# Optimization experiments

Measured on AMD Instinct MI355X. Metric: run time of the kernel, lower is better.

Reference implementation:

```python
import jax, jax.numpy as jnp
import numpy as np

NUM_HEADS = 8
MODEL_DIM = 512
HIDDEN_DIM = 64  # model_dim // num_heads
BATCH = 4
SEQ = 1024


def setup_inputs() -> dict:
    key = jax.random.key(0)
    kx, kq, kk, kv, ko = jax.random.split(key, 5)
    # xavier_uniform bound for [model_dim, hidden_dim] fan pair
    bqkv = float(np.sqrt(6.0 / (MODEL_DIM + HIDDEN_DIM)))
    bo = float(np.sqrt(6.0 / (MODEL_DIM + MODEL_DIM)))
    return {
        "X": jax.random.normal(kx, (BATCH, SEQ, MODEL_DIM), dtype=jnp.float32),
        "mask": jnp.zeros((SEQ, SEQ), dtype=bool),  # unused by module
        "Wq": jax.random.uniform(kq, (NUM_HEADS, MODEL_DIM, HIDDEN_DIM), minval=-bqkv, maxval=bqkv, dtype=jnp.float32),
        "Wk": jax.random.uniform(kk, (NUM_HEADS, MODEL_DIM, HIDDEN_DIM), minval=-bqkv, maxval=bqkv, dtype=jnp.float32),
        "Wv": jax.random.uniform(kv, (NUM_HEADS, MODEL_DIM, HIDDEN_DIM), minval=-bqkv, maxval=bqkv, dtype=jnp.float32),
        "Wo": jax.random.uniform(ko, (MODEL_DIM, MODEL_DIM), minval=-bo, maxval=bo, dtype=jnp.float32),
    }


def reference(X, mask, Wq, Wk, Wv, Wo):
    # Per-head projections (replaces the replicated-tensor lin_proj with one einsum)
    q = jnp.einsum("bsm,hmd->hbsd", X, Wq)  # [h,b,s,d]
    k = jnp.einsum("bsm,hmd->hbsd", X, Wk)
    v = jnp.einsum("bsm,hmd->hbsd", X, Wv)
    # Katharopoulos feature map on q and k
    q = jax.nn.elu(q) + 1.0
    k = jax.nn.elu(k) + 1.0
    # Cumulative outer-product state S_t = sum_{i<=t} k_i v_i^T  -> [h,b,s,d,d]
    S = jnp.cumsum(k[..., :, None] * v[..., None, :], axis=2)
    V_bar = jnp.einsum("hbsd,hbsde->hbse", q, S)  # numerator
    Z = jnp.einsum("hbsd,hbsd->hbs", q, jnp.cumsum(k, axis=2))  # normalizer
    out_heads = V_bar / Z[..., None]  # [h,b,s,d]
    # combine_heads: permute to [b,s,h,d], flatten heads, project by Wo
    b, s = out_heads.shape[1], out_heads.shape[2]
    combined = jnp.transpose(out_heads, (1, 2, 0, 3)).reshape(b, s, -1)
    return jnp.einsum("bsm,mn->bsn", combined, Wo)
```

## Files before the change

kernel.cpp:

```cpp
#include <hip/hip_runtime.h>
#include <math.h>

namespace {
typedef unsigned short u16;
typedef __attribute__((ext_vector_type(8))) short bf16x8;
typedef __attribute__((ext_vector_type(4))) float f32x4;

constexpr int H  = 8;
constexpr int B  = 4;
constexpr int S  = 1024;
constexpr int M  = 512;
constexpr int D  = 64;
constexpr int BS = B * S;
constexpr int NC = 16;
constexpr int CH = 64;
constexpr int QSZ = H * B * S * D;
constexpr int NQKV = 3 * M;

__device__ __forceinline__ float elu1(float x) {
  return x > 0.f ? x + 1.f : __expf(x);
}

__device__ __forceinline__ u16 f2bf(float f) {
  unsigned u = __builtin_bit_cast(unsigned, f);
  u += 0x7fffu + ((u >> 16) & 1u);
  return (u16)(u >> 16);
}

__device__ __forceinline__ float bf2f(u16 v) {
  return __builtin_bit_cast(float, ((unsigned)v) << 16);
}

__device__ __forceinline__ void gload16(const u16* g, u16* l) {
  __builtin_amdgcn_global_load_lds(
      (const __attribute__((address_space(1))) unsigned int*)g,
      (__attribute__((address_space(3))) unsigned int*)l, 16, 0, 0);
}

__global__ __launch_bounds__(256) void prep(
    const float* __restrict__ X, const float* __restrict__ Wq,
    const float* __restrict__ Wk, const float* __restrict__ Wv,
    const float* __restrict__ Wo, u16* __restrict__ Xb,
    u16* __restrict__ WCT, u16* __restrict__ WoT) {
  __shared__ float t[64][65];
  const int bid = blockIdx.x;
  if (bid < 2048) {
    const int i = bid * 256 + threadIdx.x;
    const float4 v = reinterpret_cast<const float4*>(X)[i];
    u16 o[4] = {f2bf(v.x), f2bf(v.y), f2bf(v.z), f2bf(v.w)};
    *reinterpret_cast<uint2*>(Xb + i * 4) = *reinterpret_cast<uint2*>(o);
  } else if (bid < 2240) {
    const int bb = bid - 2048;
    const int mt = bb & 7, ph = bb >> 3;
    const int p = ph >> 3, h = ph & 7;
    const float* W = ((p == 0) ? Wq : (p == 1) ? Wk : Wv) + h * (M * D);
    const int m0 = mt * 64;
#pragma unroll
    for (int j = 0; j < 4; ++j) {
      const int i = j * 256 + threadIdx.x;
      const int mm = i >> 4, dd = (i & 15) * 4;
      const float4 v = *reinterpret_cast<const float4*>(W + (m0 + mm) * D + dd);
      t[mm][dd + 0] = v.x; t[mm][dd + 1] = v.y;
      t[mm][dd + 2] = v.z; t[mm][dd + 3] = v.w;
    }
    __syncthreads();
    const int dd = threadIdx.x >> 2, qr = (threadIdx.x & 3) * 16;
    u16* o = WCT + (p * M + h * D + dd) * M + m0 + qr;
#pragma unroll
    for (int i = 0; i < 16; ++i) o[i] = f2bf(t[qr + i][dd]);
  } else {
    const int bb = bid - 2240;
    const int m0 = (bb & 7) * 64, n0 = (bb >> 3) * 64;
#pragma unroll
    for (int j = 0; j < 4; ++j) {
      const int i = j * 256 + threadIdx.x;
      const int mm = i >> 4, nn = (i & 15) * 4;
      const float4 v = *reinterpret_cast<const float4*>(Wo + (m0 + mm) * M + n0 + nn);
      t[mm][nn + 0] = v.x; t[mm][nn + 1] = v.y;
      t[mm][nn + 2] = v.z; t[mm][nn + 3] = v.w;
    }
    __syncthreads();
    const int nn = threadIdx.x >> 2, qr = (threadIdx.x & 3) * 16;
    u16* o = WoT + (n0 + nn) * M + m0 + qr;
#pragma unroll
    for (int i = 0; i < 16; ++i) o[i] = f2bf(t[qr + i][nn]);
  }
}

__global__ __launch_bounds__(256) void gemm_qkv(const u16* __restrict__ A,
                                                const u16* __restrict__ BT,
                                                u16* __restrict__ qb,
                                                u16* __restrict__ kb,
                                                u16* __restrict__ kTb,
                                                u16* __restrict__ vTb) {
  __shared__ alignas(16) u16 As[2][4096];
  __shared__ alignas(16) u16 Bs[2][4096];
  const int tid = threadIdx.x;
  const int wave = tid >> 6, lane = tid & 63;
  const int r0 = blockIdx.x * 128, c0 = blockIdx.y * 128;
  const int wr = (wave >> 1) * 64, wc = (wave & 1) * 64;

  f32x4 acc[4][4] = {};
  const int lrow = tid >> 2;
  const int lk = (tid & 3) * 8;
  const u16* ga0 = A + (size_t)(r0 + lrow) * 512 + lk;
  const u16* ga1 = A + (size_t)(r0 + 64 + lrow) * 512 + lk;
  const u16* gb0 = BT + (size_t)(c0 + lrow) * 512 + lk;
  const u16* gb1 = BT + (size_t)(c0 + 64 + lrow) * 512 + lk;

#define STG_QKV(kt, b)                                \
  {                                                   \
    const int ko = (kt) * 32;                         \
    gload16(ga0 + ko, &As[b][wave * 512]);            \
    gload16(ga1 + ko, &As[b][2048 + wave * 512]);     \
    gload16(gb0 + ko, &Bs[b][wave * 512]);            \
    gload16(gb1 + ko, &Bs[b][2048 + wave * 512]);     \
  }

  STG_QKV(0, 0);
  __syncthreads();
  for (int kt = 0; kt < 16; ++kt) {
    if (kt < 15) STG_QKV(kt + 1, (kt + 1) & 1);
    const bf16x8* As8 = reinterpret_cast<const bf16x8*>(As[kt & 1]);
    const bf16x8* Bs8 = reinterpret_cast<const bf16x8*>(Bs[kt & 1]);
    bf16x8 af[4], bff[4];
#pragma unroll
    for (int mf = 0; mf < 4; ++mf)
      af[mf] = As8[(wr + mf * 16 + (lane & 15)) * 4 + (lane >> 4)];
#pragma unroll
    for (int nf = 0; nf < 4; ++nf)
      bff[nf] = Bs8[(wc + nf * 16 + (lane & 15)) * 4 + (lane >> 4)];
#pragma unroll
    for (int mf = 0; mf < 4; ++mf)
#pragma unroll
      for (int nf = 0; nf < 4; ++nf)
        acc[mf][nf] = __builtin_amdgcn_mfma_f32_16x16x32_bf16(
            af[mf], bff[nf], acc[mf][nf], 0, 0, 0);
    __syncthreads();
  }
#undef STG_QKV

#pragma unroll
  for (int nf = 0; nf < 4; ++nf) {
    const int col = c0 + wc + nf * 16 + (lane & 15);
    const int p = col >> 9, hh = (col >> 6) & 7, dd = col & 63;
#pragma unroll
    for (int mf = 0; mf < 4; ++mf) {
      const int rowb = r0 + wr + mf * 16 + (lane >> 4) * 4;
      const int b = rowb >> 10, s = rowb & 1023;
      const int hb = hh * B + b;
      u16 ov[4];
#pragma unroll
      for (int r = 0; r < 4; ++r) {
        float v = acc[mf][nf][r];
        if (p < 2) v = elu1(v);
        ov[r] = f2bf(v);
      }
      if (p == 0) {
#pragma unroll
        for (int r = 0; r < 4; ++r)
          qb[((size_t)(hb << 10) + s + r) * 64 + dd] = ov[r];
      } else if (p == 1) {
#pragma unroll
        for (int r = 0; r < 4; ++r)
          kb[((size_t)(hb << 10) + s + r) * 64 + dd] = ov[r];
        *reinterpret_cast<uint2*>(kTb + ((size_t)(hb * 64 + dd) << 10) + s) =
            *reinterpret_cast<uint2*>(ov);
      } else {
        *reinterpret_cast<uint2*>(vTb + ((size_t)(hb * 64 + dd) << 10) + s) =
            *reinterpret_cast<uint2*>(ov);
      }
    }
  }
}

__global__ __launch_bounds__(256) void gemm_out(const u16* __restrict__ A,
                                                const u16* __restrict__ BT,
                                                float* __restrict__ out) {
  __shared__ alignas(16) u16 As[2][4096];
  __shared__ alignas(16) u16 Bs[2][2048];
  const int tid = threadIdx.x;
  const int wave = tid >> 6, lane = tid & 63;
  const int r0 = blockIdx.x * 128, c0 = blockIdx.y * 64;
  const int wr = (wave >> 1) * 64, wc = (wave & 1) * 32;

  f32x4 acc[4][2] = {};
  const int lrow = tid >> 2;
  const int lk = (tid & 3) * 8;
  const u16* ga0 = A + (size_t)(r0 + lrow) * 512 + lk;
  const u16* ga1 = A + (size_t)(r0 + 64 + lrow) * 512 + lk;
  const u16* gb0 = BT + (size_t)(c0 + lrow) * 512 + lk;

#define STG_OUT(kt, b)                                \
  {                                                   \
    const int ko = (kt) * 32;                         \
    gload16(ga0 + ko, &As[b][wave * 512]);            \
    gload16(ga1 + ko, &As[b][2048 + wave * 512]);     \
    if (wave < 4) gload16(gb0 + ko, &Bs[b][wave * 512]); \
  }

  STG_OUT(0, 0);
  __syncthreads();
  for (int kt = 0; kt < 16; ++kt) {
    if (kt < 15) STG_OUT(kt + 1, (kt + 1) & 1);
    const bf16x8* As8 = reinterpret_cast<const bf16x8*>(As[kt & 1]);
    const bf16x8* Bs8 = reinterpret_cast<const bf16x8*>(Bs[kt & 1]);
    bf16x8 a[4], b[2];
#pragma unroll
    for (int mf = 0; mf < 4; ++mf)
      a[mf] = As8[(wr + mf * 16 + (lane & 15)) * 4 + (lane >> 4)];
#pragma unroll
    for (int nf = 0; nf < 2; ++nf)
      b[nf] = Bs8[(wc + nf * 16 + (lane & 15)) * 4 + (lane >> 4)];
#pragma unroll
    for (int mf = 0; mf < 4; ++mf)
#pragma unroll
      for (int nf = 0; nf < 2; ++nf)
        acc[mf][nf] = __builtin_amdgcn_mfma_f32_16x16x32_bf16(
            a[mf], b[nf], acc[mf][nf], 0, 0, 0);
    __syncthreads();
  }
#undef STG_OUT

#pragma unroll
  for (int nf = 0; nf < 2; ++nf) {
    const int col = c0 + wc + nf * 16 + (lane & 15);
#pragma unroll
    for (int mf = 0; mf < 4; ++mf)
#pragma unroll
      for (int r = 0; r < 4; ++r) {
        const int row = r0 + wr + mf * 16 + (lane >> 4) * 4 + r;
        out[(size_t)row * M + col] = acc[mf][nf][r];
      }
  }
}

__global__ __launch_bounds__(256) void chunkstate_mfma(
    const u16* __restrict__ kTb, const u16* __restrict__ vTb,
    float* __restrict__ G32, float* __restrict__ Ks) {
  const int tid = threadIdx.x, wave = tid >> 6, lane = tid & 63;
  const int bx = blockIdx.x, hb = bx >> 4, cc = bx & 15, s0 = cc * CH;
  const u16* vbase = vTb + ((size_t)hb * 64) * 1024 + s0;
  const u16* kbase = kTb + ((size_t)hb * 64) * 1024 + s0;

  bf16x8 av[2];
#pragma unroll
  for (int ks = 0; ks < 2; ++ks)
    av[ks] = *reinterpret_cast<const bf16x8*>(
        vbase + (size_t)(wave * 16 + (lane & 15)) * 1024 + ks * 32 + (lane >> 4) * 8);

  f32x4 acc[4] = {};
#pragma unroll
  for (int fd = 0; fd < 4; ++fd)
#pragma unroll
    for (int ks = 0; ks < 2; ++ks) {
      bf16x8 bk = *reinterpret_cast<const bf16x8*>(
          kbase + (size_t)(fd * 16 + (lane & 15)) * 1024 + ks * 32 + (lane >> 4) * 8);
      acc[fd] = __builtin_amdgcn_mfma_f32_16x16x32_bf16(av[ks], bk, acc[fd], 0, 0, 0);
    }

  float* Gp = G32 + (size_t)bx * 4096;
#pragma unroll
  for (int fd = 0; fd < 4; ++fd)
#pragma unroll
    for (int r = 0; r < 4; ++r) {
      const int e = wave * 16 + (lane >> 4) * 4 + r;
      const int d = fd * 16 + (lane & 15);
      Gp[e * 64 + d] = acc[fd][r];
    }

  const int d = tid >> 2, tq = tid & 3;
  const u16* kp = kbase + (size_t)d * 1024 + tq * 16;
  float ks = 0.f;
#pragma unroll
  for (int j = 0; j < 16; ++j) ks += bf2f(kp[j]);
  ks += __shfl_xor(ks, 1);
  ks += __shfl_xor(ks, 2);
  if (tq == 0) Ks[bx * 64 + d] = ks;
}

__global__ __launch_bounds__(256) void prefix_kernel(
    const float* __restrict__ G32, u16* __restrict__ GTb,
    float* __restrict__ Ks) {
  const int hb = blockIdx.x, eg = blockIdx.y;
  const int tid = threadIdx.x;
  const int e = eg * 4 + (tid >> 6), d = tid & 63;
  const size_t base = ((size_t)(hb * 16) * 64 + e) * 64 + d;
  float acc = 0.f;
#pragma unroll
  for (int c = 0; c < 16; ++c) {
    const float v = G32[base + (size_t)c * 4096];
    GTb[base + (size_t)c * 4096] = f2bf(acc);
    acc += v;
  }
  if (eg == 0 && tid < 64) {
    float ka = 0.f;
#pragma unroll
    for (int c = 0; c < 16; ++c) {
      const int idx = (hb * 16 + c) * 64 + tid;
      const float v = Ks[idx];
      Ks[idx] = ka;
      ka += v;
    }
  }
}

__global__ __launch_bounds__(256) void chunkout_mfma(
    const u16* __restrict__ qb, const u16* __restrict__ kb,
    const u16* __restrict__ vTb, const u16* __restrict__ GTb,
    const float* __restrict__ Kc, u16* __restrict__ att) {
  __shared__ alignas(16) u16 Qs[4096], Kls[4096], Vs[4096], Gs[4096], Astg[4096];
  const int tid = threadIdx.x, wave = tid >> 6, lane = tid & 63;
  const int bx = blockIdx.x, hb = bx >> 4, cc = bx & 15, s0 = cc * CH;
  const int h = hb >> 2, b = hb & 3;

  {
    const u16* qg = qb + ((size_t)(hb << 10) + s0) * 64;
    const u16* kg = kb + ((size_t)(hb << 10) + s0) * 64;
    const u16* gg = GTb + (size_t)bx * 4096;
#pragma unroll
    for (int j = 0; j < 2; ++j) {
      const int off = j * 2048 + wave * 512;
      gload16(qg + off + lane * 8, Qs + off);
      gload16(kg + off + lane * 8, Kls + off);
      gload16(gg + off + lane * 8, Gs + off);
    }
    const u16* vg = vTb + ((size_t)hb * 64) * 1024 + s0;
#pragma unroll
    for (int j = 0; j < 2; ++j) {
      const int e0 = j * 32 + wave * 8;
      gload16(vg + (size_t)(e0 + (lane >> 3)) * 1024 + (lane & 7) * 8,
              Vs + e0 * 64);
    }
  }
  __syncthreads();

  const bf16x8* Qs8 = reinterpret_cast<const bf16x8*>(Qs);
  const bf16x8* Ks8 = reinterpret_cast<const bf16x8*>(Kls);
  const bf16x8* Vs8 = reinterpret_cast<const bf16x8*>(Vs);
  const bf16x8* Gs8 = reinterpret_cast<const bf16x8*>(Gs);
  const bf16x8* As8 = reinterpret_cast<const bf16x8*>(Astg);

  const int i0 = wave * 16;
  const int l15 = lane & 15, lk = lane >> 4;

  bf16x8 aq[2];
#pragma unroll
  for (int ks = 0; ks < 2; ++ks)
    aq[ks] = Qs8[(i0 + l15) * 8 + ks * 4 + lk];

  f32x4 a[4] = {};
#pragma unroll
  for (int fj = 0; fj < 4; ++fj)
#pragma unroll
    for (int ks = 0; ks < 2; ++ks) {
      bf16x8 bk = Ks8[(fj * 16 + l15) * 8 + ks * 4 + lk];
      a[fj] = __builtin_amdgcn_mfma_f32_16x16x32_bf16(aq[ks], bk, a[fj], 0, 0, 0);
    }

  const float4 kc4 = *reinterpret_cast<const float4*>(Kc + bx * 64 + l15 * 4);
  float z[4];
  const int rbase = lk * 4;
#pragma unroll
  for (int r = 0; r < 4; ++r) {
    const int il = rbase + r;
    float sum = 0.f;
#pragma unroll
    for (int fj = 0; fj < 4; ++fj) {
      const int j = fj * 16 + l15;
      if (j > i0 + il) a[fj][r] = 0.f;
      sum += a[fj][r];
    }
    const uint2 qrow = *reinterpret_cast<const uint2*>(Qs + (i0 + il) * 64 + l15 * 4);
    const u16* qr16 = reinterpret_cast<const u16*>(&qrow);
    sum += bf2f(qr16[0]) * kc4.x + bf2f(qr16[1]) * kc4.y +
           bf2f(qr16[2]) * kc4.z + bf2f(qr16[3]) * kc4.w;
    z[r] = sum;
  }
#pragma unroll
  for (int off = 1; off <= 8; off <<= 1)
#pragma unroll
    for (int r = 0; r < 4; ++r) z[r] += __shfl_xor(z[r], off);

#pragma unroll
  for (int fj = 0; fj < 4; ++fj)
#pragma unroll
    for (int r = 0; r < 4; ++r)
      Astg[(i0 + rbase + r) * 64 + fj * 16 + l15] = f2bf(a[fj][r]);

  f32x4 o[4] = {};
#pragma unroll
  for (int fe = 0; fe < 4; ++fe) {
#pragma unroll
    for (int ks = 0; ks < 2; ++ks) {
      bf16x8 bg = Gs8[(fe * 16 + l15) * 8 + ks * 4 + lk];
      o[fe] = __builtin_amdgcn_mfma_f32_16x16x32_bf16(aq[ks], bg, o[fe], 0, 0, 0);
    }
#pragma unroll
    for (int ks = 0; ks < 2; ++ks) {
      bf16x8 aa = As8[(i0 + l15) * 8 + ks * 4 + lk];
      bf16x8 bv = Vs8[(fe * 16 + l15) * 8 + ks * 4 + lk];
      o[fe] = __builtin_amdgcn_mfma_f32_16x16x32_bf16(aa, bv, o[fe], 0, 0, 0);
    }
  }

  float rz[4];
#pragma unroll
  for (int r = 0; r < 4; ++r) rz[r] = 1.f / z[r];
#pragma unroll
  for (int fe = 0; fe < 4; ++fe)
#pragma unroll
    for (int r = 0; r < 4; ++r) {
      const int srow = s0 + i0 + rbase + r;
      att[((size_t)(b << 10) + srow) * 512 + h * 64 + fe * 16 + l15] =
          f2bf(o[fe][r] * rz[r]);
    }
}

}

extern "C" void kernel_launch(void* const* d_in, const int* in_sizes, int n_in,
                              void* d_out, int out_size, void* d_ws,
                              size_t ws_size, hipStream_t stream) {
  const float* X  = (const float*)d_in[0];
  const float* Wq = (const float*)d_in[2];
  const float* Wk = (const float*)d_in[3];
  const float* Wv = (const float*)d_in[4];
  const float* Wo = (const float*)d_in[5];
  float* out = (float*)d_out;

  u16* Xb  = (u16*)d_ws;
  u16* att = Xb;
  u16* WCT = Xb + QSZ;
  u16* WoT = WCT + NQKV * M;
  u16* qb  = WoT + M * M;
  u16* kb  = qb + QSZ;
  u16* kTb = kb + QSZ;
  u16* vTb = kTb + QSZ;
  u16* GTb = vTb + QSZ;
  float* G32 = (float*)(GTb + QSZ);
  float* Ks  = G32 + QSZ;

  prep<<<dim3(2304), 256, 0, stream>>>(X, Wq, Wk, Wv, Wo, Xb, WCT, WoT);
  gemm_qkv<<<dim3(BS / 128, NQKV / 128), 256, 0, stream>>>(Xb, WCT, qb, kb,
                                                           kTb, vTb);
  chunkstate_mfma<<<dim3(H * B * NC), 256, 0, stream>>>(kTb, vTb, G32, Ks);
  prefix_kernel<<<dim3(H * B, 16), 256, 0, stream>>>(G32, GTb, Ks);
  chunkout_mfma<<<dim3(H * B * NC), 256, 0, stream>>>(qb, kb, vTb, GTb, Ks,
                                                      att);
  gemm_out<<<dim3(BS / 128, M / 64), 256, 0, stream>>>(att, WoT, out);
}
```

Before: 52.63 us.

## Fold chunk prefix sum into chunkout and widen GEMM K-tiles with swizzled LDS

Removes the separate prefix_kernel launch: chunkstate now writes per-chunk states as bf16, and each chunkout block sums the preceding chunk states and key sums itself before its main work. Both projection GEMMs switch to 64-wide K tiles with an XOR-swizzled LDS layout, halving loop iterations and reducing bank conflicts. This drops one kernel launch and the fp32 state round trip, at the cost of redundant prefix work in later chunks (up to 15 state reads per block) and extra rounding, since states are stored in bf16 before being summed.

```diff
diff --git a/kernel.cpp b/kernel.cpp
--- a/kernel.cpp
+++ b/kernel.cpp
@@ -93,60 +93,64 @@
                                                 u16* __restrict__ kb,
                                                 u16* __restrict__ kTb,
                                                 u16* __restrict__ vTb) {
-  __shared__ alignas(16) u16 As[2][4096];
-  __shared__ alignas(16) u16 Bs[2][4096];
-  const int tid = threadIdx.x;
-  const int wave = tid >> 6, lane = tid & 63;
+  __shared__ alignas(16) u16 As[2][8192];
+  __shared__ alignas(16) u16 Bs[2][8192];
+  const int tid = threadIdx.x, wave = tid >> 6, lane = tid & 63;
   const int r0 = blockIdx.x * 128, c0 = blockIdx.y * 128;
   const int wr = (wave >> 1) * 64, wc = (wave & 1) * 64;
+  const int l15 = lane & 15, lk = lane >> 4, x7 = l15 & 7;
+  const int srow = wave * 8 + (lane >> 3);
+  const int scol = (((lane & 7) ^ ((lane >> 3) & 7)) * 8);
 
   f32x4 acc[4][4] = {};
-  const int lrow = tid >> 2;
-  const int lk = (tid & 3) * 8;
-  const u16* ga0 = A + (size_t)(r0 + lrow) * 512 + lk;
-  const u16* ga1 = A + (size_t)(r0 + 64 + lrow) * 512 + lk;
-  const u16* gb0 = BT + (size_t)(c0 + lrow) * 512 + lk;
-  const u16* gb1 = BT + (size_t)(c0 + 64 + lrow) * 512 + lk;
-
-#define STG_QKV(kt, b)                                \
-  {                                                   \
-    const int ko = (kt) * 32;                         \
-    gload16(ga0 + ko, &As[b][wave * 512]);            \
-    gload16(ga1 + ko, &As[b][2048 + wave * 512]);     \
-    gload16(gb0 + ko, &Bs[b][wave * 512]);            \
-    gload16(gb1 + ko, &Bs[b][2048 + wave * 512]);     \
+
+#define STG_QKV(kt, bb)                                                     \
+  {                                                                         \
+    const int k0 = (kt) * 64;                                               \
+    for (int j = 0; j < 4; ++j) {                                           \
+      gload16(A + (size_t)(r0 + j * 32 + srow) * 512 + k0 + scol,           \
+              &As[bb][j * 2048 + wave * 512]);                              \
+      gload16(BT + (size_t)(c0 + j * 32 + srow) * 512 + k0 + scol,          \
+              &Bs[bb][j * 2048 + wave * 512]);                              \
+    }                                                                       \
   }
 
   STG_QKV(0, 0);
   __syncthreads();
-  for (int kt = 0; kt < 16; ++kt) {
-    if (kt < 15) STG_QKV(kt + 1, (kt + 1) & 1);
+  for (int kt = 0; kt < 8; ++kt) {
+    if (kt < 7) STG_QKV(kt + 1, (kt + 1) & 1);
     const bf16x8* As8 = reinterpret_cast<const bf16x8*>(As[kt & 1]);
     const bf16x8* Bs8 = reinterpret_cast<const bf16x8*>(Bs[kt & 1]);
-    bf16x8 af[4], bff[4];
+    bf16x8 af[4][2], bf_[4][2];
 #pragma unroll
     for (int mf = 0; mf < 4; ++mf)
-      af[mf] = As8[(wr + mf * 16 + (lane & 15)) * 4 + (lane >> 4)];
+#pragma unroll
+      for (int ks = 0; ks < 2; ++ks)
+        af[mf][ks] = As8[(wr + mf * 16 + l15) * 8 + ((ks * 4 + lk) ^ x7)];
 #pragma unroll
     for (int nf = 0; nf < 4; ++nf)
-      bff[nf] = Bs8[(wc + nf * 16 + (lane & 15)) * 4 + (lane >> 4)];
-#pragma unroll
-    for (int mf = 0; mf < 4; ++mf)
-#pragma unroll
-      for (int nf = 0; nf < 4; ++nf)
-        acc[mf][nf] = __builtin_amdgcn_mfma_f32_16x16x32_bf16(
-            af[mf], bff[nf], acc[mf][nf], 0, 0, 0);
+#pragma unroll
+      for (int ks = 0; ks < 2; ++ks)
+        bf_[nf][ks] = Bs8[(wc + nf * 16 + l15) * 8 + ((ks * 4 + lk) ^ x7)];
+#pragma unroll
+    for (int ks = 0; ks < 2; ++ks)
+#pragma unroll
+      for (int mf = 0; mf < 4; ++mf)
+#pragma unroll
+        for (int nf = 0; nf < 4; ++nf)
+          acc[mf][nf] = __builtin_amdgcn_mfma_f32_16x16x32_bf16(
+              af[mf][ks], bf_[nf][ks], acc[mf][nf], 0, 0, 0);
     __syncthreads();
   }
 #undef STG_QKV
 
 #pragma unroll
   for (int nf = 0; nf < 4; ++nf) {
-    const int col = c0 + wc + nf * 16 + (lane & 15);
+    const int col = c0 + wc + nf * 16 + l15;
     const int p = col >> 9, hh = (col >> 6) & 7, dd = col & 63;
 #pragma unroll
     for (int mf = 0; mf < 4; ++mf) {
-      const int rowb = r0 + wr + mf * 16 + (lane >> 4) * 4;
+      const int rowb = r0 + wr + mf * 16 + lk * 4;
       const int b = rowb >> 10, s = rowb & 1023;
       const int hb = hh * B + b;
       u16 ov[4];
@@ -177,59 +181,65 @@
 __global__ __launch_bounds__(256) void gemm_out(const u16* __restrict__ A,
                                                 const u16* __restrict__ BT,
                                                 float* __restrict__ out) {
-  __shared__ alignas(16) u16 As[2][4096];
-  __shared__ alignas(16) u16 Bs[2][2048];
-  const int tid = threadIdx.x;
-  const int wave = tid >> 6, lane = tid & 63;
+  __shared__ alignas(16) u16 As[2][8192];
+  __shared__ alignas(16) u16 Bs[2][4096];
+  const int tid = threadIdx.x, wave = tid >> 6, lane = tid & 63;
   const int r0 = blockIdx.x * 128, c0 = blockIdx.y * 64;
   const int wr = (wave >> 1) * 64, wc = (wave & 1) * 32;
+  const int l15 = lane & 15, lk = lane >> 4, x7 = l15 & 7;
+  const int srow = wave * 8 + (lane >> 3);
+  const int scol = (((lane & 7) ^ ((lane >> 3) & 7)) * 8);
 
   f32x4 acc[4][2] = {};
-  const int lrow = tid >> 2;
-  const int lk = (tid & 3) * 8;
-  const u16* ga0 = A + (size_t)(r0 + lrow) * 512 + lk;
-  const u16* ga1 = A + (size_t)(r0 + 64 + lrow) * 512 + lk;
-  const u16* gb0 = BT + (size_t)(c0 + lrow) * 512 + lk;
-
-#define STG_OUT(kt, b)                                \
-  {                                                   \
-    const int ko = (kt) * 32;                         \
-    gload16(ga0 + ko, &As[b][wave * 512]);            \
-    gload16(ga1 + ko, &As[b][2048 + wave * 512]);     \
-    if (wave < 4) gload16(gb0 + ko, &Bs[b][wave * 512]); \
+
+#define STG_OUT(kt, bb)                                                     \
+  {                                                                         \
+    const int k0 = (kt) * 64;                                               \
+    for (int j = 0; j < 4; ++j)                                             \
+      gload16(A + (size_t)(r0 + j * 32 + srow) * 512 + k0 + scol,           \
+              &As[bb][j * 2048 + wave * 512]);                              \
+    for (int j = 0; j < 2; ++j)                                             \
+      gload16(BT + (size_t)(c0 + j * 32 + srow) * 512 + k0 + scol,          \
+              &Bs[bb][j * 2048 + wave * 512]);                              \
   }
 
   STG_OUT(0, 0);
   __syncthreads();
-  for (int kt = 0; kt < 16; ++kt) {
-    if (kt < 15) STG_OUT(kt + 1, (kt + 1) & 1);
+  for (int kt = 0; kt < 8; ++kt) {
+    if (kt < 7) STG_OUT(kt + 1, (kt + 1) & 1);
     const bf16x8* As8 = reinterpret_cast<const bf16x8*>(As[kt & 1]);
     const bf16x8* Bs8 = reinterpret_cast<const bf16x8*>(Bs[kt & 1]);
-    bf16x8 a[4], b[2];
+    bf16x8 a[4][2], b[2][2];
 #pragma unroll
     for (int mf = 0; mf < 4; ++mf)
-      a[mf] = As8[(wr + mf * 16 + (lane & 15)) * 4 + (lane >> 4)];
+#pragma unroll
+      for (int ks = 0; ks < 2; ++ks)
+        a[mf][ks] = As8[(wr + mf * 16 + l15) * 8 + ((ks * 4 + lk) ^ x7)];
 #pragma unroll
     for (int nf = 0; nf < 2; ++nf)
-      b[nf] = Bs8[(wc + nf * 16 + (lane & 15)) * 4 + (lane >> 4)];
+#pragma unroll
+      for (int ks = 0; ks < 2; ++ks)
+        b[nf][ks] = Bs8[(wc + nf * 16 + l15) * 8 + ((ks * 4 + lk) ^ x7)];
+#pragma unroll
+    for (int ks = 0; ks < 2; ++ks)
+#pragma unroll
+      for (int mf = 0; mf < 4; ++mf)
+#pragma unroll
+        for (int nf = 0; nf < 2; ++nf)
+          acc[mf][nf] = __builtin_amdgcn_mfma_f32_16x16x32_bf16(
+              a[mf][ks], b[nf][ks], acc[mf][nf], 0, 0, 0);
+    __syncthreads();
+  }
+#undef STG_OUT
+
+#pragma unroll
+  for (int nf = 0; nf < 2; ++nf) {
+    const int col = c0 + wc + nf * 16 + l15;
 #pragma unroll
     for (int mf = 0; mf < 4; ++mf)
 #pragma unroll
-      for (int nf = 0; nf < 2; ++nf)
-        acc[mf][nf] = __builtin_amdgcn_mfma_f32_16x16x32_bf16(
-            a[mf], b[nf], acc[mf][nf], 0, 0, 0);
-    __syncthreads();
-  }
-#undef STG_OUT
-
-#pragma unroll
-  for (int nf = 0; nf < 2; ++nf) {
-    const int col = c0 + wc + nf * 16 + (lane & 15);
-#pragma unroll
-    for (int mf = 0; mf < 4; ++mf)
-#pragma unroll
       for (int r = 0; r < 4; ++r) {
-        const int row = r0 + wr + mf * 16 + (lane >> 4) * 4 + r;
+        const int row = r0 + wr + mf * 16 + lk * 4 + r;
         out[(size_t)row * M + col] = acc[mf][nf][r];
       }
   }
@@ -237,17 +247,18 @@
 
 __global__ __launch_bounds__(256) void chunkstate_mfma(
     const u16* __restrict__ kTb, const u16* __restrict__ vTb,
-    float* __restrict__ G32, float* __restrict__ Ks) {
+    u16* __restrict__ Gb, float* __restrict__ Ks) {
   const int tid = threadIdx.x, wave = tid >> 6, lane = tid & 63;
   const int bx = blockIdx.x, hb = bx >> 4, cc = bx & 15, s0 = cc * CH;
   const u16* vbase = vTb + ((size_t)hb * 64) * 1024 + s0;
   const u16* kbase = kTb + ((size_t)hb * 64) * 1024 + s0;
+  const int l15 = lane & 15, lk = lane >> 4;
 
   bf16x8 av[2];
 #pragma unroll
   for (int ks = 0; ks < 2; ++ks)
     av[ks] = *reinterpret_cast<const bf16x8*>(
-        vbase + (size_t)(wave * 16 + (lane & 15)) * 1024 + ks * 32 + (lane >> 4) * 8);
+        vbase + (size_t)(wave * 16 + l15) * 1024 + ks * 32 + lk * 8);
 
   f32x4 acc[4] = {};
 #pragma unroll
@@ -255,19 +266,16 @@
 #pragma unroll
     for (int ks = 0; ks < 2; ++ks) {
       bf16x8 bk = *reinterpret_cast<const bf16x8*>(
-          kbase + (size_t)(fd * 16 + (lane & 15)) * 1024 + ks * 32 + (lane >> 4) * 8);
+          kbase + (size_t)(fd * 16 + l15) * 1024 + ks * 32 + lk * 8);
       acc[fd] = __builtin_amdgcn_mfma_f32_16x16x32_bf16(av[ks], bk, acc[fd], 0, 0, 0);
     }
 
-  float* Gp = G32 + (size_t)bx * 4096;
+  u16* Gp = Gb + (size_t)bx * 4096;
 #pragma unroll
   for (int fd = 0; fd < 4; ++fd)
 #pragma unroll
-    for (int r = 0; r < 4; ++r) {
-      const int e = wave * 16 + (lane >> 4) * 4 + r;
-      const int d = fd * 16 + (lane & 15);
-      Gp[e * 64 + d] = acc[fd][r];
-    }
+    for (int r = 0; r < 4; ++r)
+      Gp[(wave * 16 + lk * 4 + r) * 64 + fd * 16 + l15] = f2bf(acc[fd][r]);
 
   const int d = tid >> 2, tq = tid & 3;
   const u16* kp = kbase + (size_t)d * 1024 + tq * 16;
@@ -279,37 +287,12 @@
   if (tq == 0) Ks[bx * 64 + d] = ks;
 }
 
-__global__ __launch_bounds__(256) void prefix_kernel(
-    const float* __restrict__ G32, u16* __restrict__ GTb,
-    float* __restrict__ Ks) {
-  const int hb = blockIdx.x, eg = blockIdx.y;
-  const int tid = threadIdx.x;
-  const int e = eg * 4 + (tid >> 6), d = tid & 63;
-  const size_t base = ((size_t)(hb * 16) * 64 + e) * 64 + d;
-  float acc = 0.f;
-#pragma unroll
-  for (int c = 0; c < 16; ++c) {
-    const float v = G32[base + (size_t)c * 4096];
-    GTb[base + (size_t)c * 4096] = f2bf(acc);
-    acc += v;
-  }
-  if (eg == 0 && tid < 64) {
-    float ka = 0.f;
-#pragma unroll
-    for (int c = 0; c < 16; ++c) {
-      const int idx = (hb * 16 + c) * 64 + tid;
-      const float v = Ks[idx];
-      Ks[idx] = ka;
-      ka += v;
-    }
-  }
-}
-
 __global__ __launch_bounds__(256) void chunkout_mfma(
     const u16* __restrict__ qb, const u16* __restrict__ kb,
-    const u16* __restrict__ vTb, const u16* __restrict__ GTb,
-    const float* __restrict__ Kc, u16* __restrict__ att) {
+    const u16* __restrict__ vTb, const u16* __restrict__ Gb,
+    const float* __restrict__ Ks, u16* __restrict__ att) {
   __shared__ alignas(16) u16 Qs[4096], Kls[4096], Vs[4096], Gs[4096], Astg[4096];
+  __shared__ float Kcs[64];
   const int tid = threadIdx.x, wave = tid >> 6, lane = tid & 63;
   const int bx = blockIdx.x, hb = bx >> 4, cc = bx & 15, s0 = cc * CH;
   const int h = hb >> 2, b = hb & 3;
@@ -317,13 +300,11 @@
   {
     const u16* qg = qb + ((size_t)(hb << 10) + s0) * 64;
     const u16* kg = kb + ((size_t)(hb << 10) + s0) * 64;
-    const u16* gg = GTb + (size_t)bx * 4096;
 #pragma unroll
     for (int j = 0; j < 2; ++j) {
       const int off = j * 2048 + wave * 512;
       gload16(qg + off + lane * 8, Qs + off);
       gload16(kg + off + lane * 8, Kls + off);
-      gload16(gg + off + lane * 8, Gs + off);
     }
     const u16* vg = vTb + ((size_t)hb * 64) * 1024 + s0;
 #pragma unroll
@@ -331,6 +312,32 @@
       const int e0 = j * 32 + wave * 8;
       gload16(vg + (size_t)(e0 + (lane >> 3)) * 1024 + (lane & 7) * 8,
               Vs + e0 * 64);
+    }
+  }
+
+  {
+    const u16* gch = Gb + (size_t)(hb * 16) * 4096;
+    float gacc[16];
+#pragma unroll
+    for (int j = 0; j < 16; ++j) gacc[j] = 0.f;
+    for (int c = 0; c < cc; ++c) {
+      const bf16x8 g0 = *reinterpret_cast<const bf16x8*>(gch + (size_t)c * 4096 + tid * 16);
+      const bf16x8 g1 = *reinterpret_cast<const bf16x8*>(gch + (size_t)c * 4096 + tid * 16 + 8);
+#pragma unroll
+      for (int j = 0; j < 8; ++j) {
+        gacc[j] += bf2f((u16)g0[j]);
+        gacc[8 + j] += bf2f((u16)g1[j]);
+      }
+    }
+    u16 gq[16];
+#pragma unroll
+    for (int j = 0; j < 16; ++j) gq[j] = f2bf(gacc[j]);
+    *reinterpret_cast<uint4*>(Gs + tid * 16) = *reinterpret_cast<uint4*>(gq);
+    *reinterpret_cast<uint4*>(Gs + tid * 16 + 8) = *reinterpret_cast<uint4*>(gq + 8);
+    if (tid < 64) {
+      float kc = 0.f;
+      for (int c = 0; c < cc; ++c) kc += Ks[(hb * 16 + c) * 64 + tid];
+      Kcs[tid] = kc;
     }
   }
   __syncthreads();
@@ -358,7 +365,7 @@
       a[fj] = __builtin_amdgcn_mfma_f32_16x16x32_bf16(aq[ks], bk, a[fj], 0, 0, 0);
     }
 
-  const float4 kc4 = *reinterpret_cast<const float4*>(Kc + bx * 64 + l15 * 4);
+  const float4 kc4 = *reinterpret_cast<const float4*>(Kcs + l15 * 4);
   float z[4];
   const int rbase = lk * 4;
 #pragma unroll
@@ -437,16 +444,14 @@
   u16* kb  = qb + QSZ;
   u16* kTb = kb + QSZ;
   u16* vTb = kTb + QSZ;
-  u16* GTb = vTb + QSZ;
-  float* G32 = (float*)(GTb + QSZ);
-  float* Ks  = G32 + QSZ;
+  u16* Gb  = vTb + QSZ;
+  float* Ks = (float*)(Gb + QSZ);
 
   prep<<<dim3(2304), 256, 0, stream>>>(X, Wq, Wk, Wv, Wo, Xb, WCT, WoT);
   gemm_qkv<<<dim3(BS / 128, NQKV / 128), 256, 0, stream>>>(Xb, WCT, qb, kb,
                                                            kTb, vTb);
-  chunkstate_mfma<<<dim3(H * B * NC), 256, 0, stream>>>(kTb, vTb, G32, Ks);
-  prefix_kernel<<<dim3(H * B, 16), 256, 0, stream>>>(G32, GTb, Ks);
-  chunkout_mfma<<<dim3(H * B * NC), 256, 0, stream>>>(qb, kb, vTb, GTb, Ks,
+  chunkstate_mfma<<<dim3(H * B * NC), 256, 0, stream>>>(kTb, vTb, Gb, Ks);
+  chunkout_mfma<<<dim3(H * B * NC), 256, 0, stream>>>(qb, kb, vTb, Gb, Ks,
                                                       att);
   gemm_out<<<dim3(BS / 128, M / 64), 256, 0, stream>>>(att, WoT, out);
 }
```

Result: slower. 55.08 us (+4.7%).

## Triple-buffer LDS staging in QKV and output GEMMs with one barrier per step

Applied to the files above, without the earlier changes.

Both GEMM kernels go from double to triple buffering in shared memory. Loads now run two k-steps ahead and each step waits on a partial vmcnt. One barrier per iteration replaces two __syncthreads, which is meant to hide global-load latency and cut synchronisation. The cost is 50% more LDS per block, which may lower occupancy. The hand-written vmcnt counts also depend on exactly how the compiler emits the async loads. The always-true wave<4 guard was also dropped.

```diff
diff --git a/kernel.cpp b/kernel.cpp
--- a/kernel.cpp
+++ b/kernel.cpp
@@ -93,8 +93,8 @@
                                                 u16* __restrict__ kb,
                                                 u16* __restrict__ kTb,
                                                 u16* __restrict__ vTb) {
-  __shared__ alignas(16) u16 As[2][4096];
-  __shared__ alignas(16) u16 Bs[2][4096];
+  __shared__ alignas(16) u16 As[3][4096];
+  __shared__ alignas(16) u16 Bs[3][4096];
   const int tid = threadIdx.x;
   const int wave = tid >> 6, lane = tid & 63;
   const int r0 = blockIdx.x * 128, c0 = blockIdx.y * 128;
@@ -108,21 +108,27 @@
   const u16* gb0 = BT + (size_t)(c0 + lrow) * 512 + lk;
   const u16* gb1 = BT + (size_t)(c0 + 64 + lrow) * 512 + lk;
 
-#define STG_QKV(kt, b)                                \
+#define STG_QKV(kt, bb)                               \
   {                                                   \
     const int ko = (kt) * 32;                         \
-    gload16(ga0 + ko, &As[b][wave * 512]);            \
-    gload16(ga1 + ko, &As[b][2048 + wave * 512]);     \
-    gload16(gb0 + ko, &Bs[b][wave * 512]);            \
-    gload16(gb1 + ko, &Bs[b][2048 + wave * 512]);     \
+    gload16(ga0 + ko, &As[bb][wave * 512]);           \
+    gload16(ga1 + ko, &As[bb][2048 + wave * 512]);    \
+    gload16(gb0 + ko, &Bs[bb][wave * 512]);           \
+    gload16(gb1 + ko, &Bs[bb][2048 + wave * 512]);    \
   }
 
   STG_QKV(0, 0);
-  __syncthreads();
+  STG_QKV(1, 1);
   for (int kt = 0; kt < 16; ++kt) {
-    if (kt < 15) STG_QKV(kt + 1, (kt + 1) & 1);
-    const bf16x8* As8 = reinterpret_cast<const bf16x8*>(As[kt & 1]);
-    const bf16x8* Bs8 = reinterpret_cast<const bf16x8*>(Bs[kt & 1]);
+    if (kt < 15) {
+      asm volatile("s_waitcnt vmcnt(4)" ::: "memory");
+    } else {
+      asm volatile("s_waitcnt vmcnt(0)" ::: "memory");
+    }
+    __builtin_amdgcn_s_barrier();
+    if (kt < 14) STG_QKV(kt + 2, (kt + 2) % 3);
+    const bf16x8* As8 = reinterpret_cast<const bf16x8*>(As[kt % 3]);
+    const bf16x8* Bs8 = reinterpret_cast<const bf16x8*>(Bs[kt % 3]);
     bf16x8 af[4], bff[4];
 #pragma unroll
     for (int mf = 0; mf < 4; ++mf)
@@ -136,7 +142,6 @@
       for (int nf = 0; nf < 4; ++nf)
         acc[mf][nf] = __builtin_amdgcn_mfma_f32_16x16x32_bf16(
             af[mf], bff[nf], acc[mf][nf], 0, 0, 0);
-    __syncthreads();
   }
 #undef STG_QKV
 
@@ -177,8 +182,8 @@
 __global__ __launch_bounds__(256) void gemm_out(const u16* __restrict__ A,
                                                 const u16* __restrict__ BT,
                                                 float* __restrict__ out) {
-  __shared__ alignas(16) u16 As[2][4096];
-  __shared__ alignas(16) u16 Bs[2][2048];
+  __shared__ alignas(16) u16 As[3][4096];
+  __shared__ alignas(16) u16 Bs[3][2048];
   const int tid = threadIdx.x;
   const int wave = tid >> 6, lane = tid & 63;
   const int r0 = blockIdx.x * 128, c0 = blockIdx.y * 64;
@@ -196,15 +201,21 @@
     const int ko = (kt) * 32;                         \
     gload16(ga0 + ko, &As[b][wave * 512]);            \
     gload16(ga1 + ko, &As[b][2048 + wave * 512]);     \
-    if (wave < 4) gload16(gb0 + ko, &Bs[b][wave * 512]); \
+    gload16(gb0 + ko, &Bs[b][wave * 512]);            \
   }
 
   STG_OUT(0, 0);
-  __syncthreads();
+  STG_OUT(1, 1);
   for (int kt = 0; kt < 16; ++kt) {
-    if (kt < 15) STG_OUT(kt + 1, (kt + 1) & 1);
-    const bf16x8* As8 = reinterpret_cast<const bf16x8*>(As[kt & 1]);
-    const bf16x8* Bs8 = reinterpret_cast<const bf16x8*>(Bs[kt & 1]);
+    if (kt < 15) {
+      asm volatile("s_waitcnt vmcnt(3)" ::: "memory");
+    } else {
+      asm volatile("s_waitcnt vmcnt(0)" ::: "memory");
+    }
+    __builtin_amdgcn_s_barrier();
+    if (kt < 14) STG_OUT(kt + 2, (kt + 2) % 3);
+    const bf16x8* As8 = reinterpret_cast<const bf16x8*>(As[kt % 3]);
+    const bf16x8* Bs8 = reinterpret_cast<const bf16x8*>(Bs[kt % 3]);
     bf16x8 a[4], b[2];
 #pragma unroll
     for (int mf = 0; mf < 4; ++mf)
@@ -218,7 +229,6 @@
       for (int nf = 0; nf < 2; ++nf)
         acc[mf][nf] = __builtin_amdgcn_mfma_f32_16x16x32_bf16(
             a[mf], b[nf], acc[mf][nf], 0, 0, 0);
-    __syncthreads();
   }
 #undef STG_OUT
 
```

Result: no change. 53.41 us (+1.5%).

## Fuse chunk-state, prefix and chunk-output kernels by recomputing prefix state per block

Applied to the files above, without the earlier changes.

Removes the separate chunk-state and prefix-scan kernels. Each output block now recomputes the running K^T V state and the K column sums over all preceding chunks with MFMA and keeps the result in shared memory. This drops two launches and the fp32/bf16 round trips of the state through global memory. In exchange, compute grows quadratically with chunk index, so late chunks do up to 15 chunk-state products and the work is unbalanced across blocks.

```diff
diff --git a/kernel.cpp b/kernel.cpp
--- a/kernel.cpp
+++ b/kernel.cpp
@@ -235,95 +235,25 @@
   }
 }
 
-__global__ __launch_bounds__(256) void chunkstate_mfma(
+__global__ __launch_bounds__(256) void chunkout_fused(
+    const u16* __restrict__ qb, const u16* __restrict__ kb,
     const u16* __restrict__ kTb, const u16* __restrict__ vTb,
-    float* __restrict__ G32, float* __restrict__ Ks) {
-  const int tid = threadIdx.x, wave = tid >> 6, lane = tid & 63;
-  const int bx = blockIdx.x, hb = bx >> 4, cc = bx & 15, s0 = cc * CH;
-  const u16* vbase = vTb + ((size_t)hb * 64) * 1024 + s0;
-  const u16* kbase = kTb + ((size_t)hb * 64) * 1024 + s0;
-
-  bf16x8 av[2];
-#pragma unroll
-  for (int ks = 0; ks < 2; ++ks)
-    av[ks] = *reinterpret_cast<const bf16x8*>(
-        vbase + (size_t)(wave * 16 + (lane & 15)) * 1024 + ks * 32 + (lane >> 4) * 8);
-
-  f32x4 acc[4] = {};
-#pragma unroll
-  for (int fd = 0; fd < 4; ++fd)
-#pragma unroll
-    for (int ks = 0; ks < 2; ++ks) {
-      bf16x8 bk = *reinterpret_cast<const bf16x8*>(
-          kbase + (size_t)(fd * 16 + (lane & 15)) * 1024 + ks * 32 + (lane >> 4) * 8);
-      acc[fd] = __builtin_amdgcn_mfma_f32_16x16x32_bf16(av[ks], bk, acc[fd], 0, 0, 0);
-    }
-
-  float* Gp = G32 + (size_t)bx * 4096;
-#pragma unroll
-  for (int fd = 0; fd < 4; ++fd)
-#pragma unroll
-    for (int r = 0; r < 4; ++r) {
-      const int e = wave * 16 + (lane >> 4) * 4 + r;
-      const int d = fd * 16 + (lane & 15);
-      Gp[e * 64 + d] = acc[fd][r];
-    }
-
-  const int d = tid >> 2, tq = tid & 3;
-  const u16* kp = kbase + (size_t)d * 1024 + tq * 16;
-  float ks = 0.f;
-#pragma unroll
-  for (int j = 0; j < 16; ++j) ks += bf2f(kp[j]);
-  ks += __shfl_xor(ks, 1);
-  ks += __shfl_xor(ks, 2);
-  if (tq == 0) Ks[bx * 64 + d] = ks;
-}
-
-__global__ __launch_bounds__(256) void prefix_kernel(
-    const float* __restrict__ G32, u16* __restrict__ GTb,
-    float* __restrict__ Ks) {
-  const int hb = blockIdx.x, eg = blockIdx.y;
-  const int tid = threadIdx.x;
-  const int e = eg * 4 + (tid >> 6), d = tid & 63;
-  const size_t base = ((size_t)(hb * 16) * 64 + e) * 64 + d;
-  float acc = 0.f;
-#pragma unroll
-  for (int c = 0; c < 16; ++c) {
-    const float v = G32[base + (size_t)c * 4096];
-    GTb[base + (size_t)c * 4096] = f2bf(acc);
-    acc += v;
-  }
-  if (eg == 0 && tid < 64) {
-    float ka = 0.f;
-#pragma unroll
-    for (int c = 0; c < 16; ++c) {
-      const int idx = (hb * 16 + c) * 64 + tid;
-      const float v = Ks[idx];
-      Ks[idx] = ka;
-      ka += v;
-    }
-  }
-}
-
-__global__ __launch_bounds__(256) void chunkout_mfma(
-    const u16* __restrict__ qb, const u16* __restrict__ kb,
-    const u16* __restrict__ vTb, const u16* __restrict__ GTb,
-    const float* __restrict__ Kc, u16* __restrict__ att) {
+    u16* __restrict__ att) {
   __shared__ alignas(16) u16 Qs[4096], Kls[4096], Vs[4096], Gs[4096], Astg[4096];
+  __shared__ float Kcs[64];
   const int tid = threadIdx.x, wave = tid >> 6, lane = tid & 63;
   const int bx = blockIdx.x, hb = bx >> 4, cc = bx & 15, s0 = cc * CH;
   const int h = hb >> 2, b = hb & 3;
+  const int l15 = lane & 15, lk = lane >> 4;
 
   {
     const u16* qg = qb + ((size_t)(hb << 10) + s0) * 64;
     const u16* kg = kb + ((size_t)(hb << 10) + s0) * 64;
-    const u16* gg = GTb + (size_t)bx * 4096;
 #pragma unroll
     for (int j = 0; j < 2; ++j) {
       const int off = j * 2048 + wave * 512;
       gload16(qg + off + lane * 8, Qs + off);
       gload16(kg + off + lane * 8, Kls + off);
-      gload16(gg + off + lane * 8, Gs + off);
     }
     const u16* vg = vTb + ((size_t)hb * 64) * 1024 + s0;
 #pragma unroll
@@ -332,6 +262,46 @@
       gload16(vg + (size_t)(e0 + (lane >> 3)) * 1024 + (lane & 7) * 8,
               Vs + e0 * 64);
     }
+  }
+
+  const u16* vbase = vTb + ((size_t)hb * 64) * 1024;
+  const u16* kbase = kTb + ((size_t)hb * 64) * 1024;
+  f32x4 P[4] = {};
+  float kcum[4] = {0.f, 0.f, 0.f, 0.f};
+  for (int c = 0; c < cc; ++c) {
+    const int sc = c * 64;
+    bf16x8 av[2];
+#pragma unroll
+    for (int ks = 0; ks < 2; ++ks)
+      av[ks] = *reinterpret_cast<const bf16x8*>(
+          vbase + (size_t)(wave * 16 + l15) * 1024 + sc + ks * 32 + lk * 8);
+#pragma unroll
+    for (int fd = 0; fd < 4; ++fd) {
+      float kp = 0.f;
+#pragma unroll
+      for (int ks = 0; ks < 2; ++ks) {
+        const bf16x8 bk = *reinterpret_cast<const bf16x8*>(
+            kbase + (size_t)(fd * 16 + l15) * 1024 + sc + ks * 32 + lk * 8);
+        P[fd] = __builtin_amdgcn_mfma_f32_16x16x32_bf16(av[ks], bk, P[fd], 0, 0, 0);
+#pragma unroll
+        for (int e = 0; e < 8; ++e) kp += bf2f((u16)bk[e]);
+      }
+      kcum[fd] += kp;
+    }
+  }
+#pragma unroll
+  for (int fd = 0; fd < 4; ++fd) {
+    kcum[fd] += __shfl_xor(kcum[fd], 16);
+    kcum[fd] += __shfl_xor(kcum[fd], 32);
+  }
+#pragma unroll
+  for (int fd = 0; fd < 4; ++fd)
+#pragma unroll
+    for (int r = 0; r < 4; ++r)
+      Gs[(wave * 16 + lk * 4 + r) * 64 + fd * 16 + l15] = f2bf(P[fd][r]);
+  if (wave == 0 && lk == 0) {
+#pragma unroll
+    for (int fd = 0; fd < 4; ++fd) Kcs[fd * 16 + l15] = kcum[fd];
   }
   __syncthreads();
 
@@ -342,7 +312,6 @@
   const bf16x8* As8 = reinterpret_cast<const bf16x8*>(Astg);
 
   const int i0 = wave * 16;
-  const int l15 = lane & 15, lk = lane >> 4;
 
   bf16x8 aq[2];
 #pragma unroll
@@ -358,7 +327,7 @@
       a[fj] = __builtin_amdgcn_mfma_f32_16x16x32_bf16(aq[ks], bk, a[fj], 0, 0, 0);
     }
 
-  const float4 kc4 = *reinterpret_cast<const float4*>(Kc + bx * 64 + l15 * 4);
+  const float4 kc4 = *reinterpret_cast<const float4*>(Kcs + l15 * 4);
   float z[4];
   const int rbase = lk * 4;
 #pragma unroll
@@ -437,16 +406,10 @@
   u16* kb  = qb + QSZ;
   u16* kTb = kb + QSZ;
   u16* vTb = kTb + QSZ;
-  u16* GTb = vTb + QSZ;
-  float* G32 = (float*)(GTb + QSZ);
-  float* Ks  = G32 + QSZ;
 
   prep<<<dim3(2304), 256, 0, stream>>>(X, Wq, Wk, Wv, Wo, Xb, WCT, WoT);
   gemm_qkv<<<dim3(BS / 128, NQKV / 128), 256, 0, stream>>>(Xb, WCT, qb, kb,
                                                            kTb, vTb);
-  chunkstate_mfma<<<dim3(H * B * NC), 256, 0, stream>>>(kTb, vTb, G32, Ks);
-  prefix_kernel<<<dim3(H * B, 16), 256, 0, stream>>>(G32, GTb, Ks);
-  chunkout_mfma<<<dim3(H * B * NC), 256, 0, stream>>>(qb, kb, vTb, GTb, Ks,
-                                                      att);
+  chunkout_fused<<<dim3(H * B * NC), 256, 0, stream>>>(qb, kb, kTb, vTb, att);
   gemm_out<<<dim3(BS / 128, M / 64), 256, 0, stream>>>(att, WoT, out);
 }
```

After: 74.27 us. 1.41x slower.
